# Kernel optimization log

Measured on AMD Instinct MI355X. Metric: run time of the kernel, lower is better.

The kernel has to match this reference:

```python
import jax, jax.numpy as jnp
import numpy as np

M = 16384      # total flat points per role (8 scenes x 2048 pts)
D = 256        # d_model
H = 4          # heads
K = 16         # knn neighbors
DFF = 1024     # 4*D
LN_EPS = 1e-5


def _ln(x, g, b):
    m = jnp.mean(x, axis=-1, keepdims=True)
    v = jnp.mean((x - m) ** 2, axis=-1, keepdims=True)
    return (x - m) / jnp.sqrt(v + LN_EPS) * g + b


def _knn_block(x, coord, ctx, ctx_coord, idx,
               Wq, Wk, Wv, Wo, g1, b1, pe_w, pe_b,
               W1, bf1, W2, bf2, g2, b2):
    # x: [M,D] query feats; ctx: [N,D] context feats; idx: [M,K] neighbor ids (-1 = invalid)
    m, d = x.shape
    k = idx.shape[1]
    dh = d // H
    valid = idx >= 0
    idx_c = jnp.where(valid, idx, 0)

    xn = _ln(x, g1, b1)
    q = (xn @ Wq).reshape(m, H, dh)                      # [M,H,dh]
    k_all = ctx @ Wk                                     # [N,D]
    v_all = ctx @ Wv                                     # [N,D]

    rel = coord[:, None, :] - ctx_coord[idx_c]           # [M,K,3]
    pe = rel @ pe_w + pe_b                               # [M,K,D] relative position encoding
    kg = (k_all[idx_c] + pe).reshape(m, k, H, dh)        # gathered keys  [M,K,H,dh]
    vg = (v_all[idx_c] + pe).reshape(m, k, H, dh)        # gathered values

    scale = jnp.asarray(1.0 / np.sqrt(dh), x.dtype)
    scores = jnp.einsum('mhd,mkhd->mhk', q, kg) * scale
    scores = jnp.where(valid[:, None, :], scores, jnp.asarray(-1e9, x.dtype))
    attn = jax.nn.softmax(scores, axis=-1)
    out = jnp.einsum('mhk,mkhd->mhd', attn, vg).reshape(m, d) @ Wo
    x = x + out
    h = jax.nn.gelu(_ln(x, g2, b2) @ W1 + bf1)
    return x + (h @ W2 + bf2)


def setup_inputs() -> dict:
    key = jax.random.key(0)
    ks = jax.random.split(key, 24)
    s = 0.02
    nblk = 2  # [0]=self(a), [1]=cross(a,b)
    inp = {
        'feat_a': jax.random.normal(ks[0], (M, D), jnp.float32),
        'coord_a': jax.random.normal(ks[1], (M, 3), jnp.float32),
        'feat_b': jax.random.normal(ks[2], (M, D), jnp.float32),
        'coord_b': jax.random.normal(ks[3], (M, 3), jnp.float32),
        'Wq': jax.random.normal(ks[4], (nblk, D, D), jnp.float32) * s,
        'Wk': jax.random.normal(ks[5], (nblk, D, D), jnp.float32) * s,
        'Wv': jax.random.normal(ks[6], (nblk, D, D), jnp.float32) * s,
        'Wo': jax.random.normal(ks[7], (nblk, D, D), jnp.float32) * s,
        'ln1_g': jnp.ones((nblk, D), jnp.float32),
        'ln1_b': jnp.zeros((nblk, D), jnp.float32),
        'pe_w': jax.random.normal(ks[8], (nblk, 3, D), jnp.float32) * s,
        'pe_b': jnp.zeros((nblk, D), jnp.float32),
        'ffn_w1': jax.random.normal(ks[9], (nblk, D, DFF), jnp.float32) * s,
        'ffn_b1': jnp.zeros((nblk, DFF), jnp.float32),
        'ffn_w2': jax.random.normal(ks[10], (nblk, DFF, D), jnp.float32) * s,
        'ffn_b2': jnp.zeros((nblk, D), jnp.float32),
        'ln2_g': jnp.ones((nblk, D), jnp.float32),
        'ln2_b': jnp.zeros((nblk, D), jnp.float32),
        'knn_a2a': jax.random.randint(ks[11], (M, K), 0, M, jnp.int64 if jax.config.jax_enable_x64 else jnp.int32),
        'knn_a2b': jax.random.randint(ks[12], (M, K), 0, M, jnp.int64 if jax.config.jax_enable_x64 else jnp.int32),
    }
    return inp


def reference(feat_a, coord_a, feat_b, coord_b,
              Wq, Wk, Wv, Wo, ln1_g, ln1_b, pe_w, pe_b,
              ffn_w1, ffn_b1, ffn_w2, ffn_b2, ln2_g, ln2_b,
              knn_a2a, knn_a2b):
    def params(i):
        return (Wq[i], Wk[i], Wv[i], Wo[i], ln1_g[i], ln1_b[i], pe_w[i], pe_b[i],
                ffn_w1[i], ffn_b1[i], ffn_w2[i], ffn_b2[i], ln2_g[i], ln2_b[i])
    # layer 'self(a)': feat[a] = block(feat[a], coord[a], knn_indexes['a2a'])
    fa = _knn_block(feat_a, coord_a, feat_a, coord_a, knn_a2a, *params(0))
    # layer 'cross(a,b)': feat[a] = block(query=feat[a], context=feat[b], knn_indexes['a2b'])
    fa = _knn_block(fa, coord_a, feat_b, coord_b, knn_a2b, *params(1))
    return fa
```

## Files before the change

kernel.cpp:

```cpp
#include <hip/hip_runtime.h>
#include <hip/hip_bf16.h>
#include <stdint.h>

#define MM 16384
#define DD 256
#define HH 4
#define KK 16
#define DFF_ 1024

typedef __attribute__((ext_vector_type(8))) short bf16x8;
typedef __attribute__((ext_vector_type(16))) float f32x16;
typedef __attribute__((ext_vector_type(2))) float f32x2;

__device__ __forceinline__ unsigned short f2bf(float f) {
    unsigned u = __builtin_bit_cast(unsigned, f);
    unsigned r = u + 0x7fffu + ((u >> 16) & 1u);
    return (unsigned short)(r >> 16);
}
__device__ __forceinline__ float bf2f(unsigned short h) {
    unsigned u = ((unsigned)h) << 16;
    return __builtin_bit_cast(float, u);
}


__global__ __launch_bounds__(256) void prep_weights(
        const float* __restrict__ Wq, const float* __restrict__ Wk,
        const float* __restrict__ Wv, const float* __restrict__ Wo,
        const float* __restrict__ W1, const float* __restrict__ W2,
        unsigned short* __restrict__ wf) {
    int t = blockIdx.x * blockDim.x + threadIdx.x;
    const float* src; unsigned short* dst;
    int kd, lg, rem, blk, e, sect;
    if (t < 131072) { sect = 0; rem = t; blk = rem >> 16; e = rem & 65535;
        src = Wq; dst = wf + blk * 65536; kd = 256; lg = 8; }
    else if (t < 262144) { sect = 1; rem = t - 131072; blk = rem >> 16; e = rem & 65535;
        src = Wk; dst = wf + 131072 + blk * 131072; kd = 256; lg = 8; }
    else if (t < 393216) { sect = 2; rem = t - 262144; blk = rem >> 16; e = rem & 65535;
        src = Wv; dst = wf + 131072 + blk * 131072; kd = 256; lg = 8; }
    else if (t < 524288) { sect = 0; rem = t - 393216; blk = rem >> 16; e = rem & 65535;
        src = Wo; dst = wf + 393216 + blk * 65536; kd = 256; lg = 8; }
    else if (t < 1048576) { sect = 0; rem = t - 524288; blk = rem >> 18; e = rem & 262143;
        src = W1; dst = wf + 524288 + blk * 262144; kd = 256; lg = 10; }
    else if (t < 1572864) { sect = 0; rem = t - 1048576; blk = rem >> 18; e = rem & 262143;
        src = W2; dst = wf + 1048576 + blk * 262144; kd = 1024; lg = 8; }
    else return;
    int k = e >> lg;
    int n = e & ((1 << lg) - 1);
    if (sect == 1) n = (n >> 2) * 8 + (n & 3);
    else if (sect == 2) n = (n >> 2) * 8 + 4 + (n & 3);
    float v = src[(size_t)blk * kd * (1 << lg) + e];
    int off = ((n >> 5) * (kd >> 4) + (k >> 4)) * 512 + (((k >> 3) & 1) * 32 + (n & 31)) * 8 + (k & 7);
    dst[off] = f2bf(v);
}

__global__ __launch_bounds__(256) void ln3_to_frag(
        const float* __restrict__ xa, const float* __restrict__ g,
        const float* __restrict__ b, const float* __restrict__ xb,
        unsigned short* __restrict__ outln, unsigned short* __restrict__ outca,
        unsigned short* __restrict__ outcb) {
    int y = blockIdx.y;
    const float* x = (y == 2) ? xb : xa;
    unsigned short* out = (y == 0) ? outln : (y == 1 ? outca : outcb);
    int apply_ln = (y == 0);
    int wave = threadIdx.x >> 6, lane = threadIdx.x & 63;
    int m = blockIdx.x * 4 + wave;
    const float4 xv = reinterpret_cast<const float4*>(x + (size_t)m * DD)[lane];
    float vals[4] = {xv.x, xv.y, xv.z, xv.w};
    int k0 = lane * 4;
    if (apply_ln) {
        float s = vals[0] + vals[1] + vals[2] + vals[3];
        float sq = vals[0]*vals[0] + vals[1]*vals[1] + vals[2]*vals[2] + vals[3]*vals[3];
        for (int o = 32; o; o >>= 1) { s += __shfl_xor(s, o, 64); sq += __shfl_xor(sq, o, 64); }
        float mean = s * (1.0f / DD);
        float var = sq * (1.0f / DD) - mean * mean;
        float rs = rsqrtf(var + 1e-5f);
        #pragma unroll
        for (int c = 0; c < 4; ++c)
            vals[c] = (vals[c] - mean) * rs * g[k0 + c] + b[k0 + c];
    }
    int chunk = ((m >> 5) * (DD >> 4) + (k0 >> 4)) * 64 + ((k0 >> 3) & 1) * 32 + (m & 31);
    ushort4 o4 = make_ushort4(f2bf(vals[0]), f2bf(vals[1]), f2bf(vals[2]), f2bf(vals[3]));
    *reinterpret_cast<ushort4*>(out + (size_t)chunk * 8 + (k0 & 7)) = o4;
}

template <int KG>
__device__ __forceinline__ void compute_tile(
        const bf16x8* __restrict__ a0, const bf16x8* __restrict__ a1,
        const bf16x8* __restrict__ b0, const bf16x8* __restrict__ b1,
        f32x16 acc[2][2]) {
    #pragma unroll 4
    for (int g = 0; g < KG; ++g) {
        bf16x8 av0 = a0[g * 64];
        bf16x8 av1 = a1[g * 64];
        bf16x8 bv0 = b0[g * 64];
        bf16x8 bv1 = b1[g * 64];
        acc[0][0] = __builtin_amdgcn_mfma_f32_32x32x16_bf16(av0, bv0, acc[0][0], 0, 0, 0);
        acc[0][1] = __builtin_amdgcn_mfma_f32_32x32x16_bf16(av0, bv1, acc[0][1], 0, 0, 0);
        acc[1][0] = __builtin_amdgcn_mfma_f32_32x32x16_bf16(av1, bv0, acc[1][0], 0, 0, 0);
        acc[1][1] = __builtin_amdgcn_mfma_f32_32x32x16_bf16(av1, bv1, acc[1][1], 0, 0, 0);
    }
}

__global__ __launch_bounds__(256) void gemm_gelu(
        const bf16x8* __restrict__ A, const bf16x8* __restrict__ B,
        unsigned short* __restrict__ outp, const float* __restrict__ bias,
        int out_kd) {
    constexpr int KG = 16;
    __shared__ float lds[4 * 1056];
    int wave = threadIdx.x >> 6, lane = threadIdx.x & 63;
    int wm = wave & 1, wn = wave >> 1;
    int id = blockIdx.x;
    int xcd = id & 7, slot = id >> 3;
    int bx = 32 * xcd + (slot & 31);
    int by = slot >> 5;
    int mw = bx * 64 + wm * 32;
    int nw = by * 128 + wn * 64;
    const bf16x8* a0 = A + ((size_t)(mw >> 5) * KG) * 64 + lane;
    const bf16x8* b0 = B + ((size_t)(nw >> 5) * KG) * 64 + lane;
    const bf16x8* b1 = b0 + (size_t)KG * 64;
    f32x16 acc[2] = {};
    #pragma unroll 4
    for (int g = 0; g < KG; ++g) {
        bf16x8 av = a0[g * 64];
        bf16x8 bv0 = b0[g * 64];
        bf16x8 bv1 = b1[g * 64];
        acc[0] = __builtin_amdgcn_mfma_f32_32x32x16_bf16(av, bv0, acc[0], 0, 0, 0);
        acc[1] = __builtin_amdgcn_mfma_f32_32x32x16_bf16(av, bv1, acc[1], 0, 0, 0);
    }
    int col = lane & 31, rq = (lane >> 5) * 4;
    float* wlds = &lds[wave * 1056];
    for (int j = 0; j < 2; ++j) {
        #pragma unroll
        for (int r = 0; r < 16; ++r) {
            int row = (r & 3) + 8 * (r >> 2) + rq;
            int n = nw + j * 32 + col;
            float v = acc[j][r] + bias[n];
            float arg = v * (1.5957691216f + 0.0713548163f * v * v);
            v = v * __frcp_rn(1.0f + __expf(-arg));
            wlds[row * 33 + col] = v;
        }
        #pragma unroll
        for (int it = 0; it < 2; ++it) {
            int task = lane + it * 64;
            int row = task >> 2, cc = task & 3;
            int m = mw + row;
            int k = nw + j * 32 + cc * 8;
            float* p = &wlds[row * 33 + cc * 8];
            unsigned short us[8];
            #pragma unroll
            for (int e = 0; e < 8; ++e) us[e] = f2bf(p[e]);
            int chunk = ((m >> 5) * (out_kd >> 4) + (k >> 4)) * 64 + ((k >> 3) & 1) * 32 + (m & 31);
            reinterpret_cast<uint4*>(outp)[chunk] = *reinterpret_cast<uint4*>(us);
        }
    }
}

template <int KD, int NOUT, bool RESID, bool BIAS>
__global__ __launch_bounds__(256) void gemm_frag64(
        const bf16x8* __restrict__ A, const bf16x8* __restrict__ B,
        float* __restrict__ outp, const float* __restrict__ resid,
        const float* __restrict__ bias) {
    constexpr int KG = KD / 16;
    int wave = threadIdx.x >> 6, lane = threadIdx.x & 63;
    int wm = wave & 1, wn = wave >> 1;
    int id = blockIdx.x;
    int xcd = id & 7, slot = id >> 3;
    int bx = 32 * xcd + (slot >> 1);
    int by = slot & 1;
    int mw = bx * 64 + wm * 32;
    int nw = by * 128 + wn * 64;
    const bf16x8* a0 = A + ((size_t)(mw >> 5) * KG) * 64 + lane;
    const bf16x8* b0 = B + ((size_t)(nw >> 5) * KG) * 64 + lane;
    const bf16x8* b1 = b0 + (size_t)KG * 64;
    f32x16 acc[2] = {};
    #pragma unroll 4
    for (int g = 0; g < KG; ++g) {
        bf16x8 av = a0[g * 64];
        bf16x8 bv0 = b0[g * 64];
        bf16x8 bv1 = b1[g * 64];
        acc[0] = __builtin_amdgcn_mfma_f32_32x32x16_bf16(av, bv0, acc[0], 0, 0, 0);
        acc[1] = __builtin_amdgcn_mfma_f32_32x32x16_bf16(av, bv1, acc[1], 0, 0, 0);
    }
    int col = lane & 31, rq = (lane >> 5) * 4;
    #pragma unroll
    for (int j = 0; j < 2; ++j) {
        #pragma unroll
        for (int r = 0; r < 16; ++r) {
            int row = (r & 3) + 8 * (r >> 2) + rq;
            int m = mw + row;
            int n = nw + j * 32 + col;
            float v = acc[j][r];
            if (BIAS) v += bias[n];
            if (RESID) v += resid[(size_t)m * NOUT + n];
            outp[(size_t)m * NOUT + n] = v;
        }
    }
}

__global__ __launch_bounds__(256) void gemm_qkv(
        const bf16x8* __restrict__ Aq, const bf16x8* __restrict__ Akv,
        const bf16x8* __restrict__ Bq, const bf16x8* __restrict__ Bkv,
        unsigned short* __restrict__ qout, unsigned char* __restrict__ kvout) {
    constexpr int KG = 16;
    int wave = threadIdx.x >> 6, lane = threadIdx.x & 63;
    int wm = wave & 1, wn = wave >> 1;
    int id = blockIdx.x;
    int xcd = id & 7, slot = id >> 3;
    int bx = 16 * xcd + (slot & 15);
    int y = slot >> 4;
    bool isQ = y < 2;
    const bf16x8* A = isQ ? Aq : Akv;
    const bf16x8* B = isQ ? Bq : Bkv;
    int n0 = (isQ ? y : y - 2) * 128 + wn * 64;
    int m0 = bx * 128 + wm * 64;
    const bf16x8* a0 = A + ((size_t)(m0 >> 5) * KG) * 64 + lane;
    const bf16x8* a1 = a0 + (size_t)KG * 64;
    const bf16x8* b0 = B + ((size_t)(n0 >> 5) * KG) * 64 + lane;
    const bf16x8* b1 = b0 + (size_t)KG * 64;
    f32x16 acc[2][2] = {};
    compute_tile<KG>(a0, a1, b0, b1, acc);
    int col = lane & 31, rq = (lane >> 5) * 4;
    #pragma unroll
    for (int i = 0; i < 2; ++i)
    #pragma unroll
    for (int j = 0; j < 2; ++j)
    #pragma unroll
    for (int r = 0; r < 16; ++r) {
        int row = (r & 3) + 8 * (r >> 2) + rq;
        int m = m0 + i * 32 + row;
        int n = n0 + j * 32 + col;
        float v = acc[i][j][r];
        if (isQ) qout[(size_t)m * 256 + n] = f2bf(v);
        else kvout[(size_t)m * 512 + n] =
            (unsigned char)(__builtin_amdgcn_cvt_pk_fp8_f32(v, v, 0, false) & 0xff);
    }
}

template <int O, int N>
__device__ __forceinline__ void redstage(float* a, int lane) {
    int sel = lane & O;
    #pragma unroll
    for (int u = 0; u < N / 2; ++u) {
        float lo = a[2 * u], hi = a[2 * u + 1];
        float keep = sel ? hi : lo;
        float send = sel ? lo : hi;
        a[u] = keep + __shfl_xor(send, O, 64);
    }
}

template <int KD, bool BIAS>
__global__ __launch_bounds__(512) void gemm_ln(
        const bf16x8* __restrict__ A, const bf16x8* __restrict__ B,
        float* __restrict__ out_f32, const float* __restrict__ resid,
        const float* __restrict__ bias,
        const float* __restrict__ lng, const float* __restrict__ lnb,
        unsigned short* __restrict__ out_frag) {
    constexpr int KG = KD / 16;
    __shared__ float pstat[4][64][2];
    __shared__ float stats[64][2];
    __shared__ float tlds[8][32 * 33];
    int wave = threadIdx.x >> 6, lane = threadIdx.x & 63;
    int wm = wave >> 2, wn = wave & 3;
    int m0 = blockIdx.x * 64;
    int mw = m0 + wm * 32;
    int n0 = wn * 64;
    const bf16x8* a0 = A + ((size_t)(mw >> 5) * KG) * 64 + lane;
    const bf16x8* b0 = B + ((size_t)(n0 >> 5) * KG) * 64 + lane;
    const bf16x8* b1 = b0 + (size_t)KG * 64;
    f32x16 acc[2] = {};
    #pragma unroll 4
    for (int g = 0; g < KG; ++g) {
        bf16x8 av = a0[g * 64];
        bf16x8 bv0 = b0[g * 64];
        bf16x8 bv1 = b1[g * 64];
        acc[0] = __builtin_amdgcn_mfma_f32_32x32x16_bf16(av, bv0, acc[0], 0, 0, 0);
        acc[1] = __builtin_amdgcn_mfma_f32_32x32x16_bf16(av, bv1, acc[1], 0, 0, 0);
    }
    int col = lane & 31, rq = (lane >> 5) * 4;

    #pragma unroll
    for (int j = 0; j < 2; ++j) {
        #pragma unroll
        for (int r = 0; r < 16; ++r) {
            int row = (r & 3) + 8 * (r >> 2) + rq;
            int m = mw + row;
            int n = n0 + j * 32 + col;
            float v = acc[j][r];
            if (BIAS) v += bias[n];
            v += resid[(size_t)m * DD + n];
            out_f32[(size_t)m * DD + n] = v;
            acc[j][r] = v;
        }
    }

    {
        float ps[16];
        #pragma unroll
        for (int r = 0; r < 16; ++r)
            ps[r] = acc[0][r] + acc[1][r];
        redstage<1, 16>(ps, lane);
        redstage<2, 8>(ps, lane);
        redstage<4, 4>(ps, lane);
        redstage<8, 2>(ps, lane);
        float sum64 = ps[0] + __shfl_xor(ps[0], 16, 64);
        float qs[16];
        #pragma unroll
        for (int r = 0; r < 16; ++r) {
            float a = acc[0][r], b = acc[1][r];
            qs[r] = a * a + b * b;
        }
        redstage<1, 16>(qs, lane);
        redstage<2, 8>(qs, lane);
        redstage<4, 4>(qs, lane);
        redstage<8, 2>(qs, lane);
        float sq64 = qs[0] + __shfl_xor(qs[0], 16, 64);
        int slot = lane & 15;
        int ROW = wm * 32 + (slot & 3) + 8 * (slot >> 2) + rq;
        if ((lane & 16) == 0)
            *reinterpret_cast<float2*>(&pstat[wn][ROW][0]) = make_float2(sum64, sq64);
    }
    __syncthreads();
    if (threadIdx.x < 64) {
        int R = threadIdx.x;
        float s = 0.0f, sq = 0.0f;
        #pragma unroll
        for (int w = 0; w < 4; ++w) {
            float2 p = *reinterpret_cast<float2*>(&pstat[w][R][0]);
            s += p.x; sq += p.y;
        }
        float mean = s * (1.0f / DD);
        float var = sq * (1.0f / DD) - mean * mean;
        float rstd = rsqrtf(var + 1e-5f);
        *reinterpret_cast<float2*>(&stats[R][0]) = make_float2(mean, rstd);
    }
    __syncthreads();

    float* wlds = &tlds[wave][0];
    float mean_r[16], rstd_r[16];
    #pragma unroll
    for (int r = 0; r < 16; ++r) {
        int row = (r & 3) + 8 * (r >> 2) + rq;
        float2 st = *reinterpret_cast<float2*>(&stats[wm * 32 + row][0]);
        mean_r[r] = st.x; rstd_r[r] = st.y;
    }
    for (int j = 0; j < 2; ++j) {
        float gj = lng[n0 + j * 32 + col];
        float bj = lnb[n0 + j * 32 + col];
        #pragma unroll
        for (int r = 0; r < 16; ++r) {
            int row = (r & 3) + 8 * (r >> 2) + rq;
            float v = (acc[j][r] - mean_r[r]) * rstd_r[r] * gj + bj;
            wlds[row * 33 + col] = v;
        }
        #pragma unroll
        for (int it = 0; it < 2; ++it) {
            int task = lane + it * 64;
            int row = task >> 2, cc = task & 3;
            int m = mw + row;
            int k = n0 + j * 32 + cc * 8;
            float* p = &wlds[row * 33 + cc * 8];
            unsigned short us[8];
            #pragma unroll
            for (int e = 0; e < 8; ++e) us[e] = f2bf(p[e]);
            int chunk = ((m >> 5) * (DD >> 4) + (k >> 4)) * 64 + ((k >> 3) & 1) * 32 + (m & 31);
            *reinterpret_cast<uint4*>(out_frag + (size_t)chunk * 8) = *reinterpret_cast<uint4*>(us);
        }
    }
}

__global__ __launch_bounds__(256) void attn_kernel(
        const unsigned short* __restrict__ q, const unsigned char* __restrict__ kv,
        const float* __restrict__ coord, const float* __restrict__ ctx_coord,
        const int* __restrict__ knn,
        const float* __restrict__ pe_w, const float* __restrict__ pe_b,
        unsigned short* __restrict__ out_frag) {
    int wave = threadIdx.x >> 6, lane = threadIdx.x & 63;
    int m = blockIdx.x * 4 + wave;
    int s = lane & 15;
    int d0 = (lane >> 4) * 64 + s * 4;

    ushort4 qv4 = *reinterpret_cast<const ushort4*>(q + (size_t)m * DD + d0);
    float qx = bf2f(qv4.x), qy = bf2f(qv4.y), qz = bf2f(qv4.z), qw = bf2f(qv4.w);
    float4 pw0 = *reinterpret_cast<const float4*>(pe_w + d0);
    float4 pw1 = *reinterpret_cast<const float4*>(pe_w + DD + d0);
    float4 pw2 = *reinterpret_cast<const float4*>(pe_w + 2 * DD + d0);
    float4 pbv = *reinterpret_cast<const float4*>(pe_b + d0);

    float cx = coord[m * 3], cy = coord[m * 3 + 1], cz = coord[m * 3 + 2];
    int myidx = knn[(size_t)m * KK + s];
    int icm = myidx < 0 ? 0 : myidx;
    float rx = cx - ctx_coord[icm * 3];
    float ry = cy - ctx_coord[icm * 3 + 1];
    float rz = cz - ctx_coord[icm * 3 + 2];

    float t0 = qx * pw0.x + qy * pw0.y + qz * pw0.z + qw * pw0.w;
    float t1 = qx * pw1.x + qy * pw1.y + qz * pw1.z + qw * pw1.w;
    float t2 = qx * pw2.x + qy * pw2.y + qz * pw2.z + qw * pw2.w;
    float t3 = qx * pbv.x + qy * pbv.y + qz * pbv.z + qw * pbv.w;
    #pragma unroll
    for (int o = 1; o < 16; o <<= 1) {
        t0 += __shfl_xor(t0, o, 64);
        t1 += __shfl_xor(t1, o, 64);
        t2 += __shfl_xor(t2, o, 64);
        t3 += __shfl_xor(t3, o, 64);
    }

    float P[KK];
    unsigned vpk[KK];
    #pragma unroll
    for (int j = 0; j < KK; ++j) {
        int ij = __shfl(myidx, j, 64);
        int ic = ij < 0 ? 0 : ij;
        uint2 kvv = *reinterpret_cast<const uint2*>(kv + (size_t)ic * 512 + (d0 >> 2) * 8);
        vpk[j] = kvv.y;
        f32x2 k01 = __builtin_amdgcn_cvt_pk_f32_fp8(kvv.x, false);
        f32x2 k23 = __builtin_amdgcn_cvt_pk_f32_fp8(kvv.x, true);
        P[j] = qx * k01.x + qy * k01.y + qz * k23.x + qw * k23.y;
    }
    redstage<1, 16>(P, lane);
    redstage<2, 8>(P, lane);
    redstage<4, 4>(P, lane);
    redstage<8, 2>(P, lane);
    float corr = rx * t0 + ry * t1 + rz * t2 + t3;
    float sc_own = (myidx >= 0) ? (P[0] + corr) * 0.125f : -1e9f;

    float mx = sc_own;
    mx = fmaxf(mx, __shfl_xor(mx, 1, 64));
    mx = fmaxf(mx, __shfl_xor(mx, 2, 64));
    mx = fmaxf(mx, __shfl_xor(mx, 4, 64));
    mx = fmaxf(mx, __shfl_xor(mx, 8, 64));
    float e = __expf(sc_own - mx);
    float sum = e;
    sum += __shfl_xor(sum, 1, 64);
    sum += __shfl_xor(sum, 2, 64);
    sum += __shfl_xor(sum, 4, 64);
    sum += __shfl_xor(sum, 8, 64);
    float w_own = e * __frcp_rn(sum);

    float wrx = w_own * rx, wry = w_own * ry, wrz = w_own * rz;
    #pragma unroll
    for (int o = 1; o < 16; o <<= 1) {
        wrx += __shfl_xor(wrx, o, 64);
        wry += __shfl_xor(wry, o, 64);
        wrz += __shfl_xor(wrz, o, 64);
    }

    int gbase = lane & 48;
    float ax = 0.f, ay = 0.f, az = 0.f, aw = 0.f;
    #pragma unroll
    for (int j = 0; j < KK; ++j) {
        float wj = __shfl(w_own, gbase + j, 64);
        f32x2 v01 = __builtin_amdgcn_cvt_pk_f32_fp8(vpk[j], false);
        f32x2 v23 = __builtin_amdgcn_cvt_pk_f32_fp8(vpk[j], true);
        ax += wj * v01.x;
        ay += wj * v01.y;
        az += wj * v23.x;
        aw += wj * v23.y;
    }
    ax += wrx * pw0.x + wry * pw1.x + wrz * pw2.x + pbv.x;
    ay += wrx * pw0.y + wry * pw1.y + wrz * pw2.y + pbv.y;
    az += wrx * pw0.z + wry * pw1.z + wrz * pw2.z + pbv.z;
    aw += wrx * pw0.w + wry * pw1.w + wrz * pw2.w + pbv.w;

    ushort4 o4 = make_ushort4(f2bf(ax), f2bf(ay), f2bf(az), f2bf(aw));
    int chunk = ((m >> 5) * (DD >> 4) + (d0 >> 4)) * 64 + ((d0 >> 3) & 1) * 32 + (m & 31);
    *reinterpret_cast<ushort4*>(out_frag + (size_t)chunk * 8 + (d0 & 7)) = o4;
}

extern "C" void kernel_launch(void* const* d_in, const int* in_sizes, int n_in,
                              void* d_out, int out_size, void* d_ws, size_t ws_size,
                              hipStream_t stream) {
    const float* feat_a = (const float*)d_in[0];
    const float* coord_a = (const float*)d_in[1];
    const float* feat_b = (const float*)d_in[2];
    const float* coord_b = (const float*)d_in[3];
    const float* Wq = (const float*)d_in[4];
    const float* Wk = (const float*)d_in[5];
    const float* Wv = (const float*)d_in[6];
    const float* Wo = (const float*)d_in[7];
    const float* ln1_g = (const float*)d_in[8];
    const float* ln1_b = (const float*)d_in[9];
    const float* pe_w = (const float*)d_in[10];
    const float* pe_b = (const float*)d_in[11];
    const float* W1 = (const float*)d_in[12];
    const float* b1 = (const float*)d_in[13];
    const float* W2 = (const float*)d_in[14];
    const float* b2 = (const float*)d_in[15];
    const float* ln2_g = (const float*)d_in[16];
    const float* ln2_b = (const float*)d_in[17];
    const int* knn_a2a = (const int*)d_in[18];
    const int* knn_a2b = (const int*)d_in[19];

    char* ws = (char*)d_ws;
    unsigned short* wfrag = (unsigned short*)ws;
    float* xmid = (float*)(ws + (4ull << 20));
    float* xout0 = (float*)(ws + (20ull << 20));
    unsigned short* qbuf = (unsigned short*)(ws + (36ull << 20));
    unsigned char* kvbuf = (unsigned char*)(ws + (52ull << 20));
    unsigned short* xnf = (unsigned short*)(ws + (68ull << 20));
    unsigned short* ctxfa = (unsigned short*)(ws + (76ull << 20));
    unsigned short* attnf = (unsigned short*)(ws + (84ull << 20));
    unsigned short* ctxfb = (unsigned short*)(ws + (92ull << 20));
    unsigned short* geluf = (unsigned short*)(ws + (36ull << 20));

    const unsigned short* WQF = wfrag;
    const unsigned short* KVF = wfrag + 131072;
    const unsigned short* WOF = wfrag + 393216;
    const unsigned short* W1F = wfrag + 524288;
    const unsigned short* W2F = wfrag + 1048576;

    prep_weights<<<(1572864 + 255) / 256, 256, 0, stream>>>(Wq, Wk, Wv, Wo, W1, W2, wfrag);

    ln3_to_frag<<<dim3(MM / 4, 3), 256, 0, stream>>>(feat_a, ln1_g, ln1_b, feat_b,
                                                     xnf, ctxfa, ctxfb);

    gemm_qkv<<<768, 256, 0, stream>>>(
        (const bf16x8*)xnf, (const bf16x8*)ctxfa,
        (const bf16x8*)WQF, (const bf16x8*)KVF, qbuf, kvbuf);

    attn_kernel<<<MM / 4, 256, 0, stream>>>(qbuf, kvbuf, coord_a, coord_a, knn_a2a,
                                            pe_w, pe_b, attnf);

    gemm_ln<256, false><<<MM / 64, 512, 0, stream>>>(
        (const bf16x8*)attnf, (const bf16x8*)WOF, xmid, feat_a, nullptr,
        ln2_g, ln2_b, xnf);

    gemm_gelu<<<2048, 256, 0, stream>>>(
        (const bf16x8*)xnf, (const bf16x8*)W1F, geluf, b1, 1024);

    gemm_ln<1024, true><<<MM / 64, 512, 0, stream>>>(
        (const bf16x8*)geluf, (const bf16x8*)W2F, xout0, xmid, b2,
        ln1_g + DD, ln1_b + DD, xnf);

    gemm_qkv<<<768, 256, 0, stream>>>(
        (const bf16x8*)xnf, (const bf16x8*)ctxfb,
        (const bf16x8*)(WQF + 65536), (const bf16x8*)(KVF + 131072), qbuf, kvbuf);

    attn_kernel<<<MM / 4, 256, 0, stream>>>(qbuf, kvbuf, coord_a, coord_b, knn_a2b,
                                            pe_w + 3 * DD, pe_b + DD, attnf);

    gemm_ln<256, false><<<MM / 64, 512, 0, stream>>>(
        (const bf16x8*)attnf, (const bf16x8*)(WOF + 65536), xmid, xout0, nullptr,
        ln2_g + DD, ln2_b + DD, xnf);

    gemm_gelu<<<2048, 256, 0, stream>>>(
        (const bf16x8*)xnf, (const bf16x8*)(W1F + 262144), geluf, b1 + DFF_, 1024);

    gemm_frag64<1024, 256, true, true><<<512, 256, 0, stream>>>(
        (const bf16x8*)geluf, (const bf16x8*)(W2F + 262144), (float*)d_out, xmid,
        b2 + DD);
}
```

Baseline: 311.3 us.

## Run FFN first GEMM in FP8 with scaled W1 and FP8 LN output

Converts W1 to FP8 with a scale of 32 during weight prep, and has the post-attention LN kernel emit its normalized activations as FP8 fragments. The first FFN GEMM then uses FP8 MFMA and unscales the accumulator before bias and GELU. The aim is to halve operand bytes and use the higher-rate FP8 matrix path for the DFF projection. The cost is lower precision in that GEMM, which may hurt accuracy against the tolerance.

```diff
diff --git a/kernel.cpp b/kernel.cpp
--- a/kernel.cpp
+++ b/kernel.cpp
@@ -29,7 +29,7 @@
         const float* __restrict__ W1, const float* __restrict__ W2,
         unsigned short* __restrict__ wf) {
     int t = blockIdx.x * blockDim.x + threadIdx.x;
-    const float* src; unsigned short* dst;
+    const float* src; unsigned short* dst = nullptr;
     int kd, lg, rem, blk, e, sect;
     if (t < 131072) { sect = 0; rem = t; blk = rem >> 16; e = rem & 65535;
         src = Wq; dst = wf + blk * 65536; kd = 256; lg = 8; }
@@ -39,8 +39,8 @@
         src = Wv; dst = wf + 131072 + blk * 131072; kd = 256; lg = 8; }
     else if (t < 524288) { sect = 0; rem = t - 393216; blk = rem >> 16; e = rem & 65535;
         src = Wo; dst = wf + 393216 + blk * 65536; kd = 256; lg = 8; }
-    else if (t < 1048576) { sect = 0; rem = t - 524288; blk = rem >> 18; e = rem & 262143;
-        src = W1; dst = wf + 524288 + blk * 262144; kd = 256; lg = 10; }
+    else if (t < 1048576) { sect = 3; rem = t - 524288; blk = rem >> 18; e = rem & 262143;
+        src = W1; kd = 256; lg = 10; }
     else if (t < 1572864) { sect = 0; rem = t - 1048576; blk = rem >> 18; e = rem & 262143;
         src = W2; dst = wf + 1048576 + blk * 262144; kd = 1024; lg = 8; }
     else return;
@@ -50,7 +50,13 @@
     else if (sect == 2) n = (n >> 2) * 8 + 4 + (n & 3);
     float v = src[(size_t)blk * kd * (1 << lg) + e];
     int off = ((n >> 5) * (kd >> 4) + (k >> 4)) * 512 + (((k >> 3) & 1) * 32 + (n & 31)) * 8 + (k & 7);
-    dst[off] = f2bf(v);
+    if (sect == 3) {
+        unsigned char* d8 = ((unsigned char*)wf) + 3145728 + blk * 262144;
+        float vs = v * 32.0f;
+        d8[off] = (unsigned char)(__builtin_amdgcn_cvt_pk_fp8_f32(vs, vs, 0, false) & 0xff);
+    } else {
+        dst[off] = f2bf(v);
+    }
 }
 
 __global__ __launch_bounds__(256) void ln3_to_frag(
@@ -101,8 +107,8 @@
     }
 }
 
-__global__ __launch_bounds__(256) void gemm_gelu(
-        const bf16x8* __restrict__ A, const bf16x8* __restrict__ B,
+__global__ __launch_bounds__(256) void gemm_gelu_f8(
+        const unsigned char* __restrict__ A8, const unsigned char* __restrict__ B8,
         unsigned short* __restrict__ outp, const float* __restrict__ bias,
         int out_kd) {
     constexpr int KG = 16;
@@ -115,17 +121,17 @@
     int by = slot >> 5;
     int mw = bx * 64 + wm * 32;
     int nw = by * 128 + wn * 64;
-    const bf16x8* a0 = A + ((size_t)(mw >> 5) * KG) * 64 + lane;
-    const bf16x8* b0 = B + ((size_t)(nw >> 5) * KG) * 64 + lane;
-    const bf16x8* b1 = b0 + (size_t)KG * 64;
+    const uint2* a0 = (const uint2*)A8 + ((size_t)(mw >> 5) * KG) * 64 + lane;
+    const uint2* b0 = (const uint2*)B8 + ((size_t)(nw >> 5) * KG) * 64 + lane;
+    const uint2* b1 = b0 + (size_t)KG * 64;
     f32x16 acc[2] = {};
     #pragma unroll 4
     for (int g = 0; g < KG; ++g) {
-        bf16x8 av = a0[g * 64];
-        bf16x8 bv0 = b0[g * 64];
-        bf16x8 bv1 = b1[g * 64];
-        acc[0] = __builtin_amdgcn_mfma_f32_32x32x16_bf16(av, bv0, acc[0], 0, 0, 0);
-        acc[1] = __builtin_amdgcn_mfma_f32_32x32x16_bf16(av, bv1, acc[1], 0, 0, 0);
+        long av  = __builtin_bit_cast(long, a0[g * 64]);
+        long bv0 = __builtin_bit_cast(long, b0[g * 64]);
+        long bv1 = __builtin_bit_cast(long, b1[g * 64]);
+        acc[0] = __builtin_amdgcn_mfma_f32_32x32x16_fp8_fp8(av, bv0, acc[0], 0, 0, 0);
+        acc[1] = __builtin_amdgcn_mfma_f32_32x32x16_fp8_fp8(av, bv1, acc[1], 0, 0, 0);
     }
     int col = lane & 31, rq = (lane >> 5) * 4;
     float* wlds = &lds[wave * 1056];
@@ -134,7 +140,7 @@
         for (int r = 0; r < 16; ++r) {
             int row = (r & 3) + 8 * (r >> 2) + rq;
             int n = nw + j * 32 + col;
-            float v = acc[j][r] + bias[n];
+            float v = acc[j][r] * (1.0f / 32.0f) + bias[n];
             float arg = v * (1.5957691216f + 0.0713548163f * v * v);
             v = v * __frcp_rn(1.0f + __expf(-arg));
             wlds[row * 33 + col] = v;
@@ -248,7 +254,7 @@
     }
 }
 
-template <int KD, bool BIAS>
+template <int KD, bool BIAS, bool FP8OUT>
 __global__ __launch_bounds__(512) void gemm_ln(
         const bf16x8* __restrict__ A, const bf16x8* __restrict__ B,
         float* __restrict__ out_f32, const float* __restrict__ resid,
@@ -359,11 +365,20 @@
             int m = mw + row;
             int k = n0 + j * 32 + cc * 8;
             float* p = &wlds[row * 33 + cc * 8];
-            unsigned short us[8];
-            #pragma unroll
-            for (int e = 0; e < 8; ++e) us[e] = f2bf(p[e]);
             int chunk = ((m >> 5) * (DD >> 4) + (k >> 4)) * 64 + ((k >> 3) & 1) * 32 + (m & 31);
-            *reinterpret_cast<uint4*>(out_frag + (size_t)chunk * 8) = *reinterpret_cast<uint4*>(us);
+            if constexpr (FP8OUT) {
+                unsigned w0 = __builtin_amdgcn_cvt_pk_fp8_f32(p[0], p[1], 0, false);
+                w0 = __builtin_amdgcn_cvt_pk_fp8_f32(p[2], p[3], w0, true);
+                unsigned w1 = __builtin_amdgcn_cvt_pk_fp8_f32(p[4], p[5], 0, false);
+                w1 = __builtin_amdgcn_cvt_pk_fp8_f32(p[6], p[7], w1, true);
+                *reinterpret_cast<uint2*>((unsigned char*)out_frag + (size_t)chunk * 8) =
+                    make_uint2(w0, w1);
+            } else {
+                unsigned short us[8];
+                #pragma unroll
+                for (int e = 0; e < 8; ++e) us[e] = f2bf(p[e]);
+                *reinterpret_cast<uint4*>(out_frag + (size_t)chunk * 8) = *reinterpret_cast<uint4*>(us);
+            }
         }
     }
 }
@@ -501,13 +516,14 @@
     unsigned short* ctxfa = (unsigned short*)(ws + (76ull << 20));
     unsigned short* attnf = (unsigned short*)(ws + (84ull << 20));
     unsigned short* ctxfb = (unsigned short*)(ws + (92ull << 20));
+    unsigned char* xnf8 = (unsigned char*)(ws + (100ull << 20));
     unsigned short* geluf = (unsigned short*)(ws + (36ull << 20));
 
     const unsigned short* WQF = wfrag;
     const unsigned short* KVF = wfrag + 131072;
     const unsigned short* WOF = wfrag + 393216;
-    const unsigned short* W1F = wfrag + 524288;
     const unsigned short* W2F = wfrag + 1048576;
+    const unsigned char* W1F8 = ((const unsigned char*)wfrag) + 3145728;
 
     prep_weights<<<(1572864 + 255) / 256, 256, 0, stream>>>(Wq, Wk, Wv, Wo, W1, W2, wfrag);
 
@@ -521,14 +537,14 @@
     attn_kernel<<<MM / 4, 256, 0, stream>>>(qbuf, kvbuf, coord_a, coord_a, knn_a2a,
                                             pe_w, pe_b, attnf);
 
-    gemm_ln<256, false><<<MM / 64, 512, 0, stream>>>(
+    gemm_ln<256, false, true><<<MM / 64, 512, 0, stream>>>(
         (const bf16x8*)attnf, (const bf16x8*)WOF, xmid, feat_a, nullptr,
-        ln2_g, ln2_b, xnf);
-
-    gemm_gelu<<<2048, 256, 0, stream>>>(
-        (const bf16x8*)xnf, (const bf16x8*)W1F, geluf, b1, 1024);
-
-    gemm_ln<1024, true><<<MM / 64, 512, 0, stream>>>(
+        ln2_g, ln2_b, (unsigned short*)xnf8);
+
+    gemm_gelu_f8<<<2048, 256, 0, stream>>>(
+        xnf8, W1F8, geluf, b1, 1024);
+
+    gemm_ln<1024, true, false><<<MM / 64, 512, 0, stream>>>(
         (const bf16x8*)geluf, (const bf16x8*)W2F, xout0, xmid, b2,
         ln1_g + DD, ln1_b + DD, xnf);
 
@@ -539,12 +555,12 @@
     attn_kernel<<<MM / 4, 256, 0, stream>>>(qbuf, kvbuf, coord_a, coord_b, knn_a2b,
                                             pe_w + 3 * DD, pe_b + DD, attnf);
 
-    gemm_ln<256, false><<<MM / 64, 512, 0, stream>>>(
+    gemm_ln<256, false, true><<<MM / 64, 512, 0, stream>>>(
         (const bf16x8*)attnf, (const bf16x8*)(WOF + 65536), xmid, xout0, nullptr,
-        ln2_g + DD, ln2_b + DD, xnf);
-
-    gemm_gelu<<<2048, 256, 0, stream>>>(
-        (const bf16x8*)xnf, (const bf16x8*)(W1F + 262144), geluf, b1 + DFF_, 1024);
+        ln2_g + DD, ln2_b + DD, (unsigned short*)xnf8);
+
+    gemm_gelu_f8<<<2048, 256, 0, stream>>>(
+        xnf8, W1F8 + 262144, geluf, b1 + DFF_, 1024);
 
     gemm_frag64<1024, 256, true, true><<<512, 256, 0, stream>>>(
         (const bf16x8*)geluf, (const bf16x8*)(W2F + 262144), (float*)d_out, xmid,
```

Result: no change. 307.5 us (-1.2%).
